# Kernel optimization log

Measured on AMD Instinct MI355X. Metric: run time of the kernel, lower is better.

## Reference

```python
import jax, jax.numpy as jnp
import numpy as np

D = 256; FF = 1024; NH = 8; NL = 4; NP = 4; DH = D // NH
SHAPES = [(64, 64), (32, 32), (16, 16), (8, 8)]
B = 4; N = sum(h * w for h, w in SHAPES)


def _ln(x, g, b, eps=1e-5):
    m = jnp.mean(x, -1, keepdims=True)
    v = jnp.var(x, -1, keepdims=True)
    return (x - m) * jax.lax.rsqrt(v + eps) * g + b


def _bilinear(v, x, y, H, W):
    # v: [B, H*W, nh, dh]; x, y: [B, Nq, nh, P] pixel coords (grid_sample, align_corners=False, zero pad)
    x0 = jnp.floor(x); y0 = jnp.floor(y)
    fx = x - x0; fy = y - y0
    x0 = x0.astype(jnp.int32); y0 = y0.astype(jnp.int32)
    dh = v.shape[-1]
    acc = 0.0
    for xi, yi, w in ((x0, y0, (1 - fx) * (1 - fy)),
                      (x0 + 1, y0, fx * (1 - fy)),
                      (x0, y0 + 1, (1 - fx) * fy),
                      (x0 + 1, y0 + 1, fx * fy)):
        valid = ((xi >= 0) & (xi < W) & (yi >= 0) & (yi < H)).astype(v.dtype)
        idx = jnp.clip(yi, 0, H - 1) * W + jnp.clip(xi, 0, W - 1)  # [B,Nq,nh,P]
        Bq, Nq, nh, P = idx.shape
        idx2 = idx.transpose(0, 1, 3, 2).reshape(Bq, Nq * P, nh, 1)
        idx2 = jnp.broadcast_to(idx2, (Bq, Nq * P, nh, dh))
        g = jnp.take_along_axis(v, idx2, axis=1)  # [B, Nq*P, nh, dh]
        g = g.reshape(Bq, Nq, P, nh, dh).transpose(0, 1, 3, 2, 4)  # [B,Nq,nh,P,dh]
        acc = acc + g * (w * valid)[..., None]
    return acc


def _msdeform(value, loc, attn, shapes):
    # value [B,N,nh,dh]; loc [B,Nq,nh,L,P,2] in [0,1]; attn [B,Nq,nh,L,P]
    out = 0.0; start = 0
    for l, (H, W) in enumerate(shapes):
        v = value[:, start:start + H * W]
        start += H * W
        x = loc[:, :, :, l, :, 0] * W - 0.5
        y = loc[:, :, :, l, :, 1] * H - 0.5
        s = _bilinear(v, x, y, H, W)  # [B,Nq,nh,P,dh]
        out = out + jnp.einsum('bqhpd,bqhp->bqhd', s, attn[:, :, :, l, :])
    return out


def _forward(src, pos, reference_points, w_value, b_value, w_off, b_off, w_attn, b_attn,
             w_out, b_out, g1, be1, w1, b1, w2, b2, g2, be2, padding_mask, shapes):
    q = src + pos
    value = src @ w_value.T + b_value
    value = jnp.where(padding_mask[..., None], 0.0, value).reshape(B, N, NH, DH)
    off = (q @ w_off.T + b_off).reshape(B, N, NH, NL, NP, 2)
    attn = jax.nn.softmax((q @ w_attn.T + b_attn).reshape(B, N, NH, NL * NP), axis=-1)
    attn = attn.reshape(B, N, NH, NL, NP)
    normalizer = jnp.array([[w, h] for h, w in shapes], jnp.float32)  # [L,2] as (W,H)
    loc = reference_points[:, :, None, :, None, :] + off / normalizer[None, None, None, :, None, :]
    a = _msdeform(value, loc, attn, shapes).reshape(B, N, D) @ w_out.T + b_out
    x = _ln(src + a, g1, be1)
    f = jax.nn.relu(x @ w1.T + b1) @ w2.T + b2
    return _ln(x + f, g2, be2)


def setup_inputs() -> dict:
    key = jax.random.key(0)
    ks = iter(jax.random.split(key, 24))
    def p(shape, scale=0.02):
        return jax.random.normal(next(ks), shape, jnp.float32) * scale
    d = {}
    d['src'] = jax.random.normal(next(ks), (B, N, D), jnp.float32)
    d['pos'] = jax.random.normal(next(ks), (B, N, D), jnp.float32)
    d['reference_points'] = jax.random.uniform(next(ks), (B, N, NL, 2), dtype=jnp.float32)
    d['w_value'] = p((D, D)); d['b_value'] = jnp.zeros((D,), jnp.float32)
    d['w_off'] = p((NH * NL * NP * 2, D), 0.001); d['b_off'] = p((NH * NL * NP * 2,), 0.1)
    d['w_attn'] = p((NH * NL * NP, D)); d['b_attn'] = jnp.zeros((NH * NL * NP,), jnp.float32)
    d['w_out'] = p((D, D)); d['b_out'] = jnp.zeros((D,), jnp.float32)
    d['g1'] = jnp.ones((D,), jnp.float32); d['be1'] = jnp.zeros((D,), jnp.float32)
    d['w1'] = p((FF, D)); d['b1'] = jnp.zeros((FF,), jnp.float32)
    d['w2'] = p((D, FF)); d['b2'] = jnp.zeros((D,), jnp.float32)
    d['g2'] = jnp.ones((D,), jnp.float32); d['be2'] = jnp.zeros((D,), jnp.float32)
    d['spatial_shapes'] = jnp.array(SHAPES, jnp.int32)
    d['level_start_index'] = jnp.array(np.cumsum([0] + [h * w for h, w in SHAPES[:-1]]), jnp.int32)
    d['padding_mask'] = jnp.zeros((B, N), bool)
    return d


def reference(src, pos, reference_points, w_value, b_value, w_off, b_off, w_attn, b_attn,
              w_out, b_out, g1, be1, w1, b1, w2, b2, g2, be2,
              spatial_shapes, level_start_index, padding_mask):
    shapes = [tuple(map(int, s)) for s in np.asarray(spatial_shapes)]  # static per-level shapes
    return _forward(src, pos, reference_points, w_value, b_value, w_off, b_off, w_attn, b_attn,
                    w_out, b_out, g1, be1, w1, b1, w2, b2, g2, be2, padding_mask, shapes)
```

## Files before the change

kernel.cpp:

```cpp
#include <hip/hip_runtime.h>

#define B_SZ   4
#define NTOK   5440
#define MTOT   (B_SZ*NTOK)
#define DMODEL 256
#define FFDIM  1024

typedef __attribute__((ext_vector_type(8))) __bf16 bf16x8;
typedef __attribute__((ext_vector_type(4))) float  f32x4;

static __device__ __forceinline__ unsigned short f2b(float f) {
    unsigned u = __builtin_bit_cast(unsigned, f);
    u = (u + 0x7FFF + ((u >> 16) & 1)) >> 16;
    return (unsigned short)u;
}
static __device__ __forceinline__ float b2f(unsigned short s) {
    return __builtin_bit_cast(float, (unsigned)s << 16);
}
static __device__ __forceinline__ float lo_bf(unsigned u) {
    return __builtin_bit_cast(float, u << 16);
}
static __device__ __forceinline__ float hi_bf(unsigned u) {
    return __builtin_bit_cast(float, u & 0xffff0000u);
}

#define GLL(gp, lp) __builtin_amdgcn_global_load_lds( \
    (const __attribute__((address_space(1))) void*)(gp), \
    (__attribute__((address_space(3))) void*)(lp), 16, 0, 0)

__global__ __launch_bounds__(256)
void qkv_gemm(const unsigned short* __restrict__ src_bf,
              const unsigned short* __restrict__ q_bf,
              const unsigned short* __restrict__ wv_b,
              const unsigned short* __restrict__ woa_b,
              const float* __restrict__ b_value,
              const float* __restrict__ b_off, const float* __restrict__ b_attn,
              const unsigned char* __restrict__ rowmask,
              unsigned short* __restrict__ value_b, unsigned short* __restrict__ oa_b)
{
    const int K = 256;
    const int y = blockIdx.x;
    const bool isv = (y < 2);
    const unsigned short* A  = isv ? src_bf : q_bf;
    const unsigned short* Wt = isv ? wv_b : woa_b;
    unsigned short* C = isv ? value_b : oa_b;
    const int ldc  = isv ? 256 : 384;
    const int col0 = (isv ? y : (y - 2)) * 128;

    __shared__ unsigned short As[128 * 32];
    __shared__ unsigned short Bs[128 * 32];
    const int tid  = threadIdx.x;
    const int lane = tid & 63;
    const int wave = tid >> 6;
    const int row0 = blockIdx.y * 128;
    const int wr = (wave >> 1) * 64, wc = (wave & 1) * 64;
    const int mrow = lane & 15, quad = lane >> 4;

    f32x4 acc[4][4] = {};
    const int ri0 = tid >> 2,            ki0 = (tid & 3) * 8;
    const int ri1 = (256 + tid) >> 2,    ki1 = ((256 + tid) & 3) * 8;
    const int lds0 = (wave * 64) * 8, lds1 = (256 + wave * 64) * 8;

    for (int k0 = 0; k0 < K; k0 += 32) {
        __syncthreads();
        GLL(A  + (size_t)(row0 + ri0) * K + k0 + ki0, &As[lds0]);
        GLL(Wt + (size_t)(col0 + ri0) * K + k0 + ki0, &Bs[lds0]);
        GLL(A  + (size_t)(row0 + ri1) * K + k0 + ki1, &As[lds1]);
        GLL(Wt + (size_t)(col0 + ri1) * K + k0 + ki1, &Bs[lds1]);
        __syncthreads();

        bf16x8 af[4], bfr[4];
        #pragma unroll
        for (int t4 = 0; t4 < 4; ++t4) {
            af[t4]  = *(const bf16x8*)&As[(wr + t4 * 16 + mrow) * 32 + quad * 8];
            bfr[t4] = *(const bf16x8*)&Bs[(wc + t4 * 16 + mrow) * 32 + quad * 8];
        }
        #pragma unroll
        for (int ti = 0; ti < 4; ++ti)
            #pragma unroll
            for (int tj = 0; tj < 4; ++tj)
                acc[ti][tj] = __builtin_amdgcn_mfma_f32_16x16x32_bf16(
                                  af[ti], bfr[tj], acc[ti][tj], 0, 0, 0);
    }

    #pragma unroll
    for (int tj = 0; tj < 4; ++tj) {
        const int col = col0 + wc + tj * 16 + mrow;
        const float bv = isv ? b_value[col] : (col < 256 ? b_off[col] : b_attn[col - 256]);
        #pragma unroll
        for (int ti = 0; ti < 4; ++ti)
            #pragma unroll
            for (int r = 0; r < 4; ++r) {
                const int row = row0 + wr + ti * 16 + quad * 4 + r;
                float v = acc[ti][tj][r] + bv;
                if (isv && rowmask[row]) v = 0.f;
                C[(size_t)row * ldc + col] = f2b(v);
            }
    }
}

__global__ __launch_bounds__(256)
void mfma_gemm(const unsigned short* __restrict__ A,
               const unsigned short* __restrict__ Wt,
               const float* __restrict__ bias,
               unsigned short* __restrict__ Cb,
               int M, int Nout, int K, int relu)
{
    __shared__ unsigned short As[128 * 32];
    __shared__ unsigned short Bs[128 * 32];
    const int tid  = threadIdx.x;
    const int lane = tid & 63;
    const int wave = tid >> 6;
    const int row0 = blockIdx.y * 128, col0 = blockIdx.x * 128;
    const int wr = (wave >> 1) * 64, wc = (wave & 1) * 64;
    const int mrow = lane & 15, quad = lane >> 4;

    f32x4 acc[4][4] = {};
    const int ri0 = tid >> 2,            ki0 = (tid & 3) * 8;
    const int ri1 = (256 + tid) >> 2,    ki1 = ((256 + tid) & 3) * 8;
    const int lds0 = (wave * 64) * 8, lds1 = (256 + wave * 64) * 8;

    for (int k0 = 0; k0 < K; k0 += 32) {
        __syncthreads();
        GLL(A  + (size_t)(row0 + ri0) * K + k0 + ki0, &As[lds0]);
        GLL(Wt + (size_t)(col0 + ri0) * K + k0 + ki0, &Bs[lds0]);
        GLL(A  + (size_t)(row0 + ri1) * K + k0 + ki1, &As[lds1]);
        GLL(Wt + (size_t)(col0 + ri1) * K + k0 + ki1, &Bs[lds1]);
        __syncthreads();

        bf16x8 af[4], bfr[4];
        #pragma unroll
        for (int t4 = 0; t4 < 4; ++t4) {
            af[t4]  = *(const bf16x8*)&As[(wr + t4 * 16 + mrow) * 32 + quad * 8];
            bfr[t4] = *(const bf16x8*)&Bs[(wc + t4 * 16 + mrow) * 32 + quad * 8];
        }
        #pragma unroll
        for (int ti = 0; ti < 4; ++ti)
            #pragma unroll
            for (int tj = 0; tj < 4; ++tj)
                acc[ti][tj] = __builtin_amdgcn_mfma_f32_16x16x32_bf16(
                                  af[ti], bfr[tj], acc[ti][tj], 0, 0, 0);
    }

    #pragma unroll
    for (int tj = 0; tj < 4; ++tj) {
        const int col = col0 + wc + tj * 16 + mrow;
        const float bv = bias[col];
        #pragma unroll
        for (int ti = 0; ti < 4; ++ti)
            #pragma unroll
            for (int r = 0; r < 4; ++r) {
                const int row = row0 + wr + ti * 16 + quad * 4 + r;
                float v = acc[ti][tj][r] + bv;
                if (relu) v = fmaxf(v, 0.f);
                Cb[(size_t)row * Nout + col] = f2b(v);
            }
    }
}

__global__ __launch_bounds__(256)
void gemm_n64(const unsigned short* __restrict__ A,
              const unsigned short* __restrict__ Wt,
              const float* __restrict__ bias,
              unsigned short* __restrict__ Cb,
              int M, int Nout, int K)
{
    __shared__ unsigned short As[128 * 32];
    __shared__ unsigned short Bs[64 * 32];
    const int tid  = threadIdx.x;
    const int lane = tid & 63;
    const int wave = tid >> 6;
    const int row0 = blockIdx.y * 128, col0 = blockIdx.x * 64;
    const int wr = wave * 32;
    const int mrow = lane & 15, quad = lane >> 4;

    f32x4 acc[2][4] = {};
    const int ri0 = tid >> 2,            ki0 = (tid & 3) * 8;
    const int ri1 = (256 + tid) >> 2,    ki1 = ((256 + tid) & 3) * 8;
    const int ldsA0 = (wave * 64) * 8, ldsA1 = (256 + wave * 64) * 8;
    const int ldsB  = (wave * 64) * 8;

    for (int k0 = 0; k0 < K; k0 += 32) {
        __syncthreads();
        GLL(A  + (size_t)(row0 + ri0) * K + k0 + ki0, &As[ldsA0]);
        GLL(A  + (size_t)(row0 + ri1) * K + k0 + ki1, &As[ldsA1]);
        GLL(Wt + (size_t)(col0 + ri0) * K + k0 + ki0, &Bs[ldsB]);
        __syncthreads();

        bf16x8 af[2], bfr[4];
        #pragma unroll
        for (int ti = 0; ti < 2; ++ti)
            af[ti] = *(const bf16x8*)&As[(wr + ti * 16 + mrow) * 32 + quad * 8];
        #pragma unroll
        for (int tj = 0; tj < 4; ++tj)
            bfr[tj] = *(const bf16x8*)&Bs[(tj * 16 + mrow) * 32 + quad * 8];
        #pragma unroll
        for (int ti = 0; ti < 2; ++ti)
            #pragma unroll
            for (int tj = 0; tj < 4; ++tj)
                acc[ti][tj] = __builtin_amdgcn_mfma_f32_16x16x32_bf16(
                                  af[ti], bfr[tj], acc[ti][tj], 0, 0, 0);
    }

    #pragma unroll
    for (int tj = 0; tj < 4; ++tj) {
        const int col = col0 + tj * 16 + mrow;
        const float bv = bias[col];
        #pragma unroll
        for (int ti = 0; ti < 2; ++ti)
            #pragma unroll
            for (int r = 0; r < 4; ++r) {
                const int row = row0 + wr + ti * 16 + quad * 4 + r;
                Cb[(size_t)row * Nout + col] = f2b(acc[ti][tj][r] + bv);
            }
    }
}

__global__ __launch_bounds__(256)
void addln_kernel(const unsigned short* __restrict__ c,
                  const float* __restrict__ resid_f,
                  const unsigned short* __restrict__ resid_b,
                  const float* __restrict__ g, const float* __restrict__ be,
                  float* __restrict__ out_f, unsigned short* __restrict__ out_b)
{
    const int wave = threadIdx.x >> 6;
    const int lane = threadIdx.x & 63;
    const int row  = blockIdx.x * 4 + wave;
    const size_t base = (size_t)row * 256 + (lane << 2);

    const ushort4 cu = *(const ushort4*)(c + base);
    float4 v;
    v.x = b2f(cu.x); v.y = b2f(cu.y); v.z = b2f(cu.z); v.w = b2f(cu.w);
    if (resid_f) {
        const float4 r = *(const float4*)(resid_f + base);
        v.x += r.x; v.y += r.y; v.z += r.z; v.w += r.w;
    } else {
        const ushort4 r = *(const ushort4*)(resid_b + base);
        v.x += b2f(r.x); v.y += b2f(r.y); v.z += b2f(r.z); v.w += b2f(r.w);
    }

    float s  = v.x + v.y + v.z + v.w;
    float ss = v.x * v.x + v.y * v.y + v.z * v.z + v.w * v.w;
    #pragma unroll
    for (int off = 32; off; off >>= 1) {
        s  += __shfl_xor(s, off, 64);
        ss += __shfl_xor(ss, off, 64);
    }
    const float mean = s * (1.f / 256.f);
    const float var  = ss * (1.f / 256.f) - mean * mean;
    const float rstd = rsqrtf(var + 1e-5f);

    const float4 gv = *(const float4*)(g  + (lane << 2));
    const float4 bv = *(const float4*)(be + (lane << 2));
    float4 o;
    o.x = (v.x - mean) * rstd * gv.x + bv.x;
    o.y = (v.y - mean) * rstd * gv.y + bv.y;
    o.z = (v.z - mean) * rstd * gv.z + bv.z;
    o.w = (v.w - mean) * rstd * gv.w + bv.w;
    if (out_f) *(float4*)(out_f + base) = o;
    if (out_b) {
        ushort4 u; u.x = f2b(o.x); u.y = f2b(o.y); u.z = f2b(o.z); u.w = f2b(o.w);
        *(ushort4*)(out_b + base) = u;
    }
}

__global__ __launch_bounds__(256)
void sampling_kernel(const unsigned short* __restrict__ value,
                     const unsigned short* __restrict__ oa,
                     const float* __restrict__ refp,
                     unsigned short* __restrict__ samp)
{
    __shared__ unsigned s_pk[64 * 68];
    const int t0  = blockIdx.x * 8;
    const int tid = threadIdx.x;

    #pragma unroll
    for (int rep = 0; rep < 4; ++rep) {
        const int e   = rep * 256 + tid;
        const int tok = e >> 7;
        const int hp  = e & 127;
        const int h   = hp >> 4, i16 = hp & 15, l = i16 >> 2;
        const int t   = t0 + tok;

        const float ex = __expf(b2f(oa[(size_t)t * 384 + 256 + h * 16 + i16]));
        float ssum = ex;
        #pragma unroll
        for (int o = 8; o; o >>= 1) ssum += __shfl_xor(ssum, o, 16);
        const float aw = ex / ssum;

        const int   Wl_t[4]  = {64, 32, 16, 8};
        const int   LST_t[4] = {0, 4096, 5120, 5376};
        const int   Wl  = Wl_t[l];
        const int   LST = LST_t[l];
        const float fW  = (float)Wl;

        const unsigned ov = *(const unsigned*)&oa[(size_t)t * 384 + h * 32 + i16 * 2];
        const float ox = lo_bf(ov), oy = hi_bf(ov);
        const float2 rxy = *(const float2*)&refp[(size_t)t * 8 + l * 2];
        const float x = rxy.x * fW + ox - 0.5f;
        const float y = rxy.y * fW + oy - 0.5f;
        const float x0 = floorf(x), y0 = floorf(y);
        const float fx = x - x0, fy = y - y0;
        const int   ix = (int)x0, iy = (int)y0;
        const bool  vx0 = (ix >= 0) & (ix < Wl), vx1 = (ix + 1 >= 0) & (ix + 1 < Wl);

        const int base = (tok * 8 + h) * 68 + i16 * 4;
        #pragma unroll
        for (int j = 0; j < 2; ++j) {
            const int  yv = iy + j;
            const bool vy = (yv >= 0) & (yv < Wl);
            const float wy = (j ? fy : 1.f - fy) * aw;
            const int  rowi = LST + yv * Wl;
            const float w0 = (vy & vx0) ? wy * (1.f - fx) : 0.f;
            const float w1 = (vy & vx1) ? wy * fx : 0.f;
            const unsigned i0 = (vy & vx0) ? (unsigned)(rowi + ix) : 0u;
            const unsigned i1 = (vy & vx1) ? (unsigned)(rowi + ix + 1) : 0u;
            s_pk[base + j * 2 + 0] = (i0 << 16) | f2b(w0);
            s_pk[base + j * 2 + 1] = (i1 << 16) | f2b(w1);
        }
    }
    __syncthreads();

    const int wv_  = tid >> 6;
    const int lane = tid & 63;
    const int t2   = lane >> 5;
    const int h    = (lane >> 2) & 7;
    const int dq   = lane & 3;
    const int tok  = wv_ * 2 + t2;
    const int t    = t0 + tok;
    const int b    = t / NTOK;
    const char* vb = (const char*)value + ((size_t)b * NTOK * 256 + h * 32 + dq * 8) * 2;
    const unsigned* sp = s_pk + (tok * 8 + h) * 68;

    float a0 = 0.f, a1 = 0.f, a2 = 0.f, a3 = 0.f;
    float a4 = 0.f, a5 = 0.f, a6 = 0.f, a7 = 0.f;

    unsigned pkc = sp[0];
    uint4 vc = *(const uint4*)(vb + (size_t)(pkc >> 16) * 512);
    #pragma unroll 8
    for (int i = 0; i < 64; ++i) {
        unsigned pkn = 0; uint4 vn = make_uint4(0, 0, 0, 0);
        if (i < 63) {
            pkn = sp[i + 1];
            vn = *(const uint4*)(vb + (size_t)(pkn >> 16) * 512);
        }
        const float w = lo_bf(pkc);
        a0 += lo_bf(vc.x) * w; a1 += hi_bf(vc.x) * w;
        a2 += lo_bf(vc.y) * w; a3 += hi_bf(vc.y) * w;
        a4 += lo_bf(vc.z) * w; a5 += hi_bf(vc.z) * w;
        a6 += lo_bf(vc.w) * w; a7 += hi_bf(vc.w) * w;
        pkc = pkn; vc = vn;
    }
    ushort4 o0, o1;
    o0.x = f2b(a0); o0.y = f2b(a1); o0.z = f2b(a2); o0.w = f2b(a3);
    o1.x = f2b(a4); o1.y = f2b(a5); o1.z = f2b(a6); o1.w = f2b(a7);
    unsigned short* op = samp + (size_t)t * 256 + h * 32 + dq * 8;
    *(ushort4*)(op)     = o0;
    *(ushort4*)(op + 4) = o1;
}

__global__ __launch_bounds__(256)
void prep_kernel(const float* __restrict__ src, const float* __restrict__ pos,
                 const float* __restrict__ wv, const float* __restrict__ woff,
                 const float* __restrict__ wattn, const float* __restrict__ wout,
                 const float* __restrict__ w1, const float* __restrict__ w2,
                 unsigned short* __restrict__ q_bf, unsigned short* __restrict__ src_bf,
                 unsigned short* __restrict__ wv_b, unsigned short* __restrict__ woa_b,
                 unsigned short* __restrict__ wout_b,
                 unsigned short* __restrict__ w1_b, unsigned short* __restrict__ w2_b)
{
    const int v = blockIdx.x * 256 + threadIdx.x;
    if (v < 1392640) {
        const float4 s = ((const float4*)src)[v];
        const float4 p = ((const float4*)pos)[v];
        ushort4 qo, so;
        qo.x = f2b(s.x + p.x); qo.y = f2b(s.y + p.y);
        qo.z = f2b(s.z + p.z); qo.w = f2b(s.w + p.w);
        so.x = f2b(s.x); so.y = f2b(s.y); so.z = f2b(s.z); so.w = f2b(s.w);
        ((ushort4*)q_bf)[v]   = qo;
        ((ushort4*)src_bf)[v] = so;
        return;
    }
    const int v2 = v - 1392640;
    const float* s; unsigned short* d; int off;
    if      (v2 <  16384) { s = wv;    d = wv_b;          off = v2; }
    else if (v2 <  32768) { s = woff;  d = woa_b;         off = v2 - 16384; }
    else if (v2 <  40960) { s = wattn; d = woa_b + 65536; off = v2 - 32768; }
    else if (v2 <  57344) { s = wout;  d = wout_b;        off = v2 - 40960; }
    else if (v2 < 122880) { s = w1;    d = w1_b;          off = v2 - 57344; }
    else                  { s = w2;    d = w2_b;          off = v2 - 122880; }
    const float4 f = ((const float4*)s)[off];
    ushort4 u; u.x = f2b(f.x); u.y = f2b(f.y); u.z = f2b(f.z); u.w = f2b(f.w);
    ((ushort4*)d)[off] = u;
}

extern "C" void kernel_launch(void* const* d_in, const int* in_sizes, int n_in,
                              void* d_out, int out_size, void* d_ws, size_t ws_size,
                              hipStream_t stream) {
    const float* src     = (const float*)d_in[0];
    const float* pos     = (const float*)d_in[1];
    const float* refp    = (const float*)d_in[2];
    const float* w_value = (const float*)d_in[3];
    const float* b_value = (const float*)d_in[4];
    const float* w_off   = (const float*)d_in[5];
    const float* b_off   = (const float*)d_in[6];
    const float* w_attn  = (const float*)d_in[7];
    const float* b_attn  = (const float*)d_in[8];
    const float* w_out   = (const float*)d_in[9];
    const float* b_out   = (const float*)d_in[10];
    const float* g1      = (const float*)d_in[11];
    const float* be1     = (const float*)d_in[12];
    const float* w1      = (const float*)d_in[13];
    const float* b1      = (const float*)d_in[14];
    const float* w2      = (const float*)d_in[15];
    const float* b2      = (const float*)d_in[16];
    const float* g2      = (const float*)d_in[17];
    const float* be2     = (const float*)d_in[18];
    const unsigned char* pmask = (const unsigned char*)d_in[21];

    char* ws = (char*)d_ws;
    const size_t SZ16 = (size_t)MTOT * 256 * 2;
    unsigned short* q_bf    = (unsigned short*)(ws);
    unsigned short* src_bf  = (unsigned short*)(ws + SZ16);
    unsigned short* value_b = (unsigned short*)(ws + 2 * SZ16);
    unsigned short* oa_b    = (unsigned short*)(ws + 3 * SZ16);
    unsigned short* samp    = (unsigned short*)(ws + 3 * SZ16 + SZ16 * 3 / 2);
    unsigned short* h_bf    = (unsigned short*)(ws + 5 * SZ16 + SZ16 * 3 / 2);
    unsigned short* wts     = (unsigned short*)(ws + 9 * SZ16 + SZ16 * 3 / 2);
    unsigned short* C1_bf   = (unsigned short*)(ws + 2 * SZ16);
    unsigned short* x_bf    = (unsigned short*)(ws);
    unsigned short* C2_bf   = samp;

    unsigned short* wv_b    = wts;
    unsigned short* woa_b   = wv_b   + 65536;
    unsigned short* wout_b  = woa_b  + 98304;
    unsigned short* w1_b    = wout_b + 65536;
    unsigned short* w2_b    = w1_b   + 262144;

    const dim3 blk(256);

    prep_kernel<<<dim3(6176), blk, 0, stream>>>(src, pos, w_value, w_off, w_attn,
                                                w_out, w1, w2, q_bf, src_bf,
                                                wv_b, woa_b, wout_b, w1_b, w2_b);
    qkv_gemm<<<dim3(5, MTOT / 128), blk, 0, stream>>>(
        src_bf, q_bf, wv_b, woa_b, b_value, b_off, b_attn, pmask, value_b, oa_b);
    sampling_kernel<<<dim3(MTOT / 8), blk, 0, stream>>>(value_b, oa_b, refp, samp);
    gemm_n64<<<dim3(4, MTOT / 128), blk, 0, stream>>>(
        samp, wout_b, b_out, C1_bf, MTOT, DMODEL, DMODEL);
    addln_kernel<<<dim3(MTOT / 4), blk, 0, stream>>>(
        C1_bf, src, nullptr, g1, be1, nullptr, x_bf);
    mfma_gemm<<<dim3(FFDIM / 128, MTOT / 128), blk, 0, stream>>>(
        x_bf, w1_b, b1, h_bf, MTOT, FFDIM, DMODEL, 1);
    gemm_n64<<<dim3(4, MTOT / 128), blk, 0, stream>>>(
        h_bf, w2_b, b2, C2_bf, MTOT, DMODEL, FFDIM);
    addln_kernel<<<dim3(MTOT / 4), blk, 0, stream>>>(
        C2_bf, nullptr, x_bf, g2, be2, (float*)d_out, nullptr);
}
```

Baseline: 279.4 us.

## Remap GEMM blocks per XCD, double K-step per barrier, vectorize epilogue stores

All three GEMM kernels now use a 1D grid whose block IDs are remapped so that blocks on the same XCD share row panels. This is meant to improve L2 reuse of the A tiles. Each barrier pair now loads two 32-wide K slices into two LDS buffers, halving the number of syncs per K. The MFMA operands are swapped so each lane holds four consecutive columns, which lets the epilogue do vectorized float4 bias loads and ushort4 stores instead of scalar strided stores. The price is double the LDS use and hardcoded shapes: mfma_gemm always applies ReLU and gemm_n64 assumes 256 output columns.

```diff
diff --git a/kernel.cpp b/kernel.cpp
--- a/kernel.cpp
+++ b/kernel.cpp
@@ -5,6 +5,7 @@
 #define MTOT   (B_SZ*NTOK)
 #define DMODEL 256
 #define FFDIM  1024
+#define NROWP  (MTOT/128)
 
 typedef __attribute__((ext_vector_type(8))) __bf16 bf16x8;
 typedef __attribute__((ext_vector_type(4))) float  f32x4;
@@ -39,20 +40,25 @@
               unsigned short* __restrict__ value_b, unsigned short* __restrict__ oa_b)
 {
     const int K = 256;
-    const int y = blockIdx.x;
-    const bool isv = (y < 2);
+    const int id  = blockIdx.x;
+    const int xcd = id & 7;
+    const int j   = id >> 3;
+    const int c   = j % 5;
+    const int r   = 8 * (j / 5) + xcd;
+    if (r >= NROWP) return;
+    const int row0 = r * 128;
+    const bool isv = (c < 2);
     const unsigned short* A  = isv ? src_bf : q_bf;
     const unsigned short* Wt = isv ? wv_b : woa_b;
     unsigned short* C = isv ? value_b : oa_b;
     const int ldc  = isv ? 256 : 384;
-    const int col0 = (isv ? y : (y - 2)) * 128;
-
-    __shared__ unsigned short As[128 * 32];
-    __shared__ unsigned short Bs[128 * 32];
+    const int col0 = (isv ? c : (c - 2)) * 128;
+
+    __shared__ unsigned short As[2][128 * 32];
+    __shared__ unsigned short Bs[2][128 * 32];
     const int tid  = threadIdx.x;
     const int lane = tid & 63;
     const int wave = tid >> 6;
-    const int row0 = blockIdx.y * 128;
     const int wr = (wave >> 1) * 64, wc = (wave & 1) * 64;
     const int mrow = lane & 15, quad = lane >> 4;
 
@@ -61,41 +67,51 @@
     const int ri1 = (256 + tid) >> 2,    ki1 = ((256 + tid) & 3) * 8;
     const int lds0 = (wave * 64) * 8, lds1 = (256 + wave * 64) * 8;
 
-    for (int k0 = 0; k0 < K; k0 += 32) {
+    for (int k0 = 0; k0 < K; k0 += 64) {
         __syncthreads();
-        GLL(A  + (size_t)(row0 + ri0) * K + k0 + ki0, &As[lds0]);
-        GLL(Wt + (size_t)(col0 + ri0) * K + k0 + ki0, &Bs[lds0]);
-        GLL(A  + (size_t)(row0 + ri1) * K + k0 + ki1, &As[lds1]);
-        GLL(Wt + (size_t)(col0 + ri1) * K + k0 + ki1, &Bs[lds1]);
+        #pragma unroll
+        for (int s = 0; s < 2; ++s) {
+            const int kk = k0 + s * 32;
+            GLL(A  + (size_t)(row0 + ri0) * K + kk + ki0, &As[s][lds0]);
+            GLL(Wt + (size_t)(col0 + ri0) * K + kk + ki0, &Bs[s][lds0]);
+            GLL(A  + (size_t)(row0 + ri1) * K + kk + ki1, &As[s][lds1]);
+            GLL(Wt + (size_t)(col0 + ri1) * K + kk + ki1, &Bs[s][lds1]);
+        }
         __syncthreads();
-
-        bf16x8 af[4], bfr[4];
-        #pragma unroll
-        for (int t4 = 0; t4 < 4; ++t4) {
-            af[t4]  = *(const bf16x8*)&As[(wr + t4 * 16 + mrow) * 32 + quad * 8];
-            bfr[t4] = *(const bf16x8*)&Bs[(wc + t4 * 16 + mrow) * 32 + quad * 8];
-        }
-        #pragma unroll
-        for (int ti = 0; ti < 4; ++ti)
-            #pragma unroll
-            for (int tj = 0; tj < 4; ++tj)
-                acc[ti][tj] = __builtin_amdgcn_mfma_f32_16x16x32_bf16(
-                                  af[ti], bfr[tj], acc[ti][tj], 0, 0, 0);
+        #pragma unroll
+        for (int s = 0; s < 2; ++s) {
+            bf16x8 af[4], bfr[4];
+            #pragma unroll
+            for (int t4 = 0; t4 < 4; ++t4) {
+                af[t4]  = *(const bf16x8*)&As[s][(wr + t4 * 16 + mrow) * 32 + quad * 8];
+                bfr[t4] = *(const bf16x8*)&Bs[s][(wc + t4 * 16 + mrow) * 32 + quad * 8];
+            }
+            #pragma unroll
+            for (int ti = 0; ti < 4; ++ti)
+                #pragma unroll
+                for (int tj = 0; tj < 4; ++tj)
+                    acc[ti][tj] = __builtin_amdgcn_mfma_f32_16x16x32_bf16(
+                                      bfr[tj], af[ti], acc[ti][tj], 0, 0, 0);
+        }
     }
 
     #pragma unroll
-    for (int tj = 0; tj < 4; ++tj) {
-        const int col = col0 + wc + tj * 16 + mrow;
-        const float bv = isv ? b_value[col] : (col < 256 ? b_off[col] : b_attn[col - 256]);
-        #pragma unroll
-        for (int ti = 0; ti < 4; ++ti)
-            #pragma unroll
-            for (int r = 0; r < 4; ++r) {
-                const int row = row0 + wr + ti * 16 + quad * 4 + r;
-                float v = acc[ti][tj][r] + bv;
-                if (isv && rowmask[row]) v = 0.f;
-                C[(size_t)row * ldc + col] = f2b(v);
-            }
+    for (int ti = 0; ti < 4; ++ti) {
+        const int row = row0 + wr + ti * 16 + mrow;
+        const bool msk = isv && rowmask[row];
+        #pragma unroll
+        for (int tj = 0; tj < 4; ++tj) {
+            const int col = col0 + wc + tj * 16 + quad * 4;
+            const float4 bv = isv ? *(const float4*)(b_value + col)
+                            : (col < 256 ? *(const float4*)(b_off + col)
+                                         : *(const float4*)(b_attn + col - 256));
+            ushort4 o;
+            o.x = msk ? 0 : f2b(acc[ti][tj][0] + bv.x);
+            o.y = msk ? 0 : f2b(acc[ti][tj][1] + bv.y);
+            o.z = msk ? 0 : f2b(acc[ti][tj][2] + bv.z);
+            o.w = msk ? 0 : f2b(acc[ti][tj][3] + bv.w);
+            *(ushort4*)(C + (size_t)row * ldc + col) = o;
+        }
     }
 }
 
@@ -104,14 +120,22 @@
                const unsigned short* __restrict__ Wt,
                const float* __restrict__ bias,
                unsigned short* __restrict__ Cb,
-               int M, int Nout, int K, int relu)
+               int Nout, int K)
 {
-    __shared__ unsigned short As[128 * 32];
-    __shared__ unsigned short Bs[128 * 32];
+    const int id  = blockIdx.x;
+    const int xcd = id & 7;
+    const int j   = id >> 3;
+    const int ncol = Nout / 128;
+    const int c   = j % ncol;
+    const int r   = 8 * (j / ncol) + xcd;
+    if (r >= NROWP) return;
+    const int row0 = r * 128, col0 = c * 128;
+
+    __shared__ unsigned short As[2][128 * 32];
+    __shared__ unsigned short Bs[2][128 * 32];
     const int tid  = threadIdx.x;
     const int lane = tid & 63;
     const int wave = tid >> 6;
-    const int row0 = blockIdx.y * 128, col0 = blockIdx.x * 128;
     const int wr = (wave >> 1) * 64, wc = (wave & 1) * 64;
     const int mrow = lane & 15, quad = lane >> 4;
 
@@ -120,41 +144,48 @@
     const int ri1 = (256 + tid) >> 2,    ki1 = ((256 + tid) & 3) * 8;
     const int lds0 = (wave * 64) * 8, lds1 = (256 + wave * 64) * 8;
 
-    for (int k0 = 0; k0 < K; k0 += 32) {
+    for (int k0 = 0; k0 < K; k0 += 64) {
         __syncthreads();
-        GLL(A  + (size_t)(row0 + ri0) * K + k0 + ki0, &As[lds0]);
-        GLL(Wt + (size_t)(col0 + ri0) * K + k0 + ki0, &Bs[lds0]);
-        GLL(A  + (size_t)(row0 + ri1) * K + k0 + ki1, &As[lds1]);
-        GLL(Wt + (size_t)(col0 + ri1) * K + k0 + ki1, &Bs[lds1]);
+        #pragma unroll
+        for (int s = 0; s < 2; ++s) {
+            const int kk = k0 + s * 32;
+            GLL(A  + (size_t)(row0 + ri0) * K + kk + ki0, &As[s][lds0]);
+            GLL(Wt + (size_t)(col0 + ri0) * K + kk + ki0, &Bs[s][lds0]);
+            GLL(A  + (size_t)(row0 + ri1) * K + kk + ki1, &As[s][lds1]);
+            GLL(Wt + (size_t)(col0 + ri1) * K + kk + ki1, &Bs[s][lds1]);
+        }
         __syncthreads();
-
-        bf16x8 af[4], bfr[4];
-        #pragma unroll
-        for (int t4 = 0; t4 < 4; ++t4) {
-            af[t4]  = *(const bf16x8*)&As[(wr + t4 * 16 + mrow) * 32 + quad * 8];
-            bfr[t4] = *(const bf16x8*)&Bs[(wc + t4 * 16 + mrow) * 32 + quad * 8];
-        }
-        #pragma unroll
-        for (int ti = 0; ti < 4; ++ti)
-            #pragma unroll
-            for (int tj = 0; tj < 4; ++tj)
-                acc[ti][tj] = __builtin_amdgcn_mfma_f32_16x16x32_bf16(
-                                  af[ti], bfr[tj], acc[ti][tj], 0, 0, 0);
+        #pragma unroll
+        for (int s = 0; s < 2; ++s) {
+            bf16x8 af[4], bfr[4];
+            #pragma unroll
+            for (int t4 = 0; t4 < 4; ++t4) {
+                af[t4]  = *(const bf16x8*)&As[s][(wr + t4 * 16 + mrow) * 32 + quad * 8];
+                bfr[t4] = *(const bf16x8*)&Bs[s][(wc + t4 * 16 + mrow) * 32 + quad * 8];
+            }
+            #pragma unroll
+            for (int ti = 0; ti < 4; ++ti)
+                #pragma unroll
+                for (int tj = 0; tj < 4; ++tj)
+                    acc[ti][tj] = __builtin_amdgcn_mfma_f32_16x16x32_bf16(
+                                      bfr[tj], af[ti], acc[ti][tj], 0, 0, 0);
+        }
     }
 
     #pragma unroll
-    for (int tj = 0; tj < 4; ++tj) {
-        const int col = col0 + wc + tj * 16 + mrow;
-        const float bv = bias[col];
-        #pragma unroll
-        for (int ti = 0; ti < 4; ++ti)
-            #pragma unroll
-            for (int r = 0; r < 4; ++r) {
-                const int row = row0 + wr + ti * 16 + quad * 4 + r;
-                float v = acc[ti][tj][r] + bv;
-                if (relu) v = fmaxf(v, 0.f);
-                Cb[(size_t)row * Nout + col] = f2b(v);
-            }
+    for (int ti = 0; ti < 4; ++ti) {
+        const int row = row0 + wr + ti * 16 + mrow;
+        #pragma unroll
+        for (int tj = 0; tj < 4; ++tj) {
+            const int col = col0 + wc + tj * 16 + quad * 4;
+            const float4 bv = *(const float4*)(bias + col);
+            ushort4 o;
+            o.x = f2b(fmaxf(acc[ti][tj][0] + bv.x, 0.f));
+            o.y = f2b(fmaxf(acc[ti][tj][1] + bv.y, 0.f));
+            o.z = f2b(fmaxf(acc[ti][tj][2] + bv.z, 0.f));
+            o.w = f2b(fmaxf(acc[ti][tj][3] + bv.w, 0.f));
+            *(ushort4*)(Cb + (size_t)row * Nout + col) = o;
+        }
     }
 }
 
@@ -163,14 +194,21 @@
               const unsigned short* __restrict__ Wt,
               const float* __restrict__ bias,
               unsigned short* __restrict__ Cb,
-              int M, int Nout, int K)
+              int K)
 {
-    __shared__ unsigned short As[128 * 32];
-    __shared__ unsigned short Bs[64 * 32];
+    const int id  = blockIdx.x;
+    const int xcd = id & 7;
+    const int j   = id >> 3;
+    const int c   = j % 4;
+    const int r   = 8 * (j / 4) + xcd;
+    if (r >= NROWP) return;
+    const int row0 = r * 128, col0 = c * 64;
+
+    __shared__ unsigned short As[2][128 * 32];
+    __shared__ unsigned short Bs[2][64 * 32];
     const int tid  = threadIdx.x;
     const int lane = tid & 63;
     const int wave = tid >> 6;
-    const int row0 = blockIdx.y * 128, col0 = blockIdx.x * 64;
     const int wr = wave * 32;
     const int mrow = lane & 15, quad = lane >> 4;
 
@@ -180,39 +218,48 @@
     const int ldsA0 = (wave * 64) * 8, ldsA1 = (256 + wave * 64) * 8;
     const int ldsB  = (wave * 64) * 8;
 
-    for (int k0 = 0; k0 < K; k0 += 32) {
+    for (int k0 = 0; k0 < K; k0 += 64) {
         __syncthreads();
-        GLL(A  + (size_t)(row0 + ri0) * K + k0 + ki0, &As[ldsA0]);
-        GLL(A  + (size_t)(row0 + ri1) * K + k0 + ki1, &As[ldsA1]);
-        GLL(Wt + (size_t)(col0 + ri0) * K + k0 + ki0, &Bs[ldsB]);
+        #pragma unroll
+        for (int s = 0; s < 2; ++s) {
+            const int kk = k0 + s * 32;
+            GLL(A  + (size_t)(row0 + ri0) * K + kk + ki0, &As[s][ldsA0]);
+            GLL(A  + (size_t)(row0 + ri1) * K + kk + ki1, &As[s][ldsA1]);
+            GLL(Wt + (size_t)(col0 + ri0) * K + kk + ki0, &Bs[s][ldsB]);
+        }
         __syncthreads();
-
-        bf16x8 af[2], bfr[4];
-        #pragma unroll
-        for (int ti = 0; ti < 2; ++ti)
-            af[ti] = *(const bf16x8*)&As[(wr + ti * 16 + mrow) * 32 + quad * 8];
-        #pragma unroll
-        for (int tj = 0; tj < 4; ++tj)
-            bfr[tj] = *(const bf16x8*)&Bs[(tj * 16 + mrow) * 32 + quad * 8];
-        #pragma unroll
-        for (int ti = 0; ti < 2; ++ti)
+        #pragma unroll
+        for (int s = 0; s < 2; ++s) {
+            bf16x8 af[2], bfr[4];
+            #pragma unroll
+            for (int ti = 0; ti < 2; ++ti)
+                af[ti] = *(const bf16x8*)&As[s][(wr + ti * 16 + mrow) * 32 + quad * 8];
             #pragma unroll
             for (int tj = 0; tj < 4; ++tj)
-                acc[ti][tj] = __builtin_amdgcn_mfma_f32_16x16x32_bf16(
-                                  af[ti], bfr[tj], acc[ti][tj], 0, 0, 0);
+                bfr[tj] = *(const bf16x8*)&Bs[s][(tj * 16 + mrow) * 32 + quad * 8];
+            #pragma unroll
+            for (int ti = 0; ti < 2; ++ti)
+                #pragma unroll
+                for (int tj = 0; tj < 4; ++tj)
+                    acc[ti][tj] = __builtin_amdgcn_mfma_f32_16x16x32_bf16(
+                                      bfr[tj], af[ti], acc[ti][tj], 0, 0, 0);
+        }
     }
 
     #pragma unroll
-    for (int tj = 0; tj < 4; ++tj) {
-        const int col = col0 + tj * 16 + mrow;
-        const float bv = bias[col];
-        #pragma unroll
-        for (int ti = 0; ti < 2; ++ti)
-            #pragma unroll
-            for (int r = 0; r < 4; ++r) {
-                const int row = row0 + wr + ti * 16 + quad * 4 + r;
-                Cb[(size_t)row * Nout + col] = f2b(acc[ti][tj][r] + bv);
-            }
+    for (int ti = 0; ti < 2; ++ti) {
+        const int row = row0 + wr + ti * 16 + mrow;
+        #pragma unroll
+        for (int tj = 0; tj < 4; ++tj) {
+            const int col = col0 + tj * 16 + quad * 4;
+            const float4 bv = *(const float4*)(bias + col);
+            ushort4 o;
+            o.x = f2b(acc[ti][tj][0] + bv.x);
+            o.y = f2b(acc[ti][tj][1] + bv.y);
+            o.z = f2b(acc[ti][tj][2] + bv.z);
+            o.w = f2b(acc[ti][tj][3] + bv.w);
+            *(ushort4*)(Cb + (size_t)row * 256 + col) = o;
+        }
     }
 }
 
@@ -442,17 +489,17 @@
     prep_kernel<<<dim3(6176), blk, 0, stream>>>(src, pos, w_value, w_off, w_attn,
                                                 w_out, w1, w2, q_bf, src_bf,
                                                 wv_b, woa_b, wout_b, w1_b, w2_b);
-    qkv_gemm<<<dim3(5, MTOT / 128), blk, 0, stream>>>(
+    qkv_gemm<<<dim3(8 * 5 * 22), blk, 0, stream>>>(
         src_bf, q_bf, wv_b, woa_b, b_value, b_off, b_attn, pmask, value_b, oa_b);
     sampling_kernel<<<dim3(MTOT / 8), blk, 0, stream>>>(value_b, oa_b, refp, samp);
-    gemm_n64<<<dim3(4, MTOT / 128), blk, 0, stream>>>(
-        samp, wout_b, b_out, C1_bf, MTOT, DMODEL, DMODEL);
+    gemm_n64<<<dim3(8 * 4 * 22), blk, 0, stream>>>(
+        samp, wout_b, b_out, C1_bf, DMODEL);
     addln_kernel<<<dim3(MTOT / 4), blk, 0, stream>>>(
         C1_bf, src, nullptr, g1, be1, nullptr, x_bf);
-    mfma_gemm<<<dim3(FFDIM / 128, MTOT / 128), blk, 0, stream>>>(
-        x_bf, w1_b, b1, h_bf, MTOT, FFDIM, DMODEL, 1);
-    gemm_n64<<<dim3(4, MTOT / 128), blk, 0, stream>>>(
-        h_bf, w2_b, b2, C2_bf, MTOT, DMODEL, FFDIM);
+    mfma_gemm<<<dim3(8 * 8 * 22), blk, 0, stream>>>(
+        x_bf, w1_b, b1, h_bf, FFDIM, DMODEL);
+    gemm_n64<<<dim3(8 * 4 * 22), blk, 0, stream>>>(
+        h_bf, w2_b, b2, C2_bf, FFDIM);
     addln_kernel<<<dim3(MTOT / 4), blk, 0, stream>>>(
         C2_bf, nullptr, x_bf, g2, be2, (float*)d_out, nullptr);
 }
```

After: 273.7 us. 2.0% less time.
